# Performance work log

Hardware: AMD Instinct MI355X
Metric: run time of the kernel (lower is better)

Reference implementation:

```python
import jax, jax.numpy as jnp
import numpy as np

# Normalized wavelength grid for the 5 satellite bands (412.5, 442.5, 490, 510, 555 nm)
LAM_N = (jnp.array([412.5, 442.5, 490.0, 510.0, 555.0], dtype=jnp.float32) - 440.0) / 100.0
B1, B2, EPS, LR = 0.9, 0.999, 1e-8, 0.02  # Adam hyperparameters (torch defaults + lr)


def _optics(ch, pf):
    # ch: (B,3) log-concentrations [chla, nap, cdom]; pf: (14,) perturbation factors
    chla = jnp.exp(ch[:, 0:1])
    nap = jnp.exp(ch[:, 1:2])
    cdom = jnp.exp(ch[:, 2:3])
    a_ph = pf[0] * 0.05 * (1.0 + pf[1] * 0.1 * LAM_N + pf[2] * 0.01)       # (5,)
    a_cdom = pf[5] * 0.1 * jnp.exp(-pf[6] * 1.7 * LAM_N)                   # (5,)
    a = 0.0045 + a_ph * chla + a_cdom * cdom + pf[12] * 0.005 * nap        # (B,5)
    bb = 0.0012 + pf[3] * 0.001 * chla * (1.0 + pf[4] * 0.05 * LAM_N) + pf[13] * 0.005 * nap
    return a, bb


def _rrs(ch, X, pf):
    # Quadratic-in-u remote sensing reflectance model, modulated by direct/diffuse light split.
    a, bb = _optics(ch, pf)
    Edir, Edif = X[:, :, 0], X[:, :, 1]
    u = bb / (a + bb)
    rrs = (pf[7] * 0.089 + pf[8] * 0.1245 * u) * u
    return rrs * (Edir + 0.5 * Edif) / (Edir + Edif)  # (B,5)


def _kd(ch, X, pf):
    a, bb = _optics(ch, pf)
    mu = 0.5 + 0.5 * jax.nn.sigmoid(X[:, :, 3])  # mean cosine from zenith channel
    return (a + bb) / mu * (pf[9] * 0.9 + pf[10] * 0.1)  # (B,5)


def _bbp(ch, pf):
    chla = jnp.exp(ch[:, 0:1])
    nap = jnp.exp(ch[:, 1:2])
    lam3 = LAM_N[jnp.array([1, 2, 4])]  # bbp reported at 442.5, 490, 555 nm
    return pf[11] * (pf[3] * 0.001 * chla * (1.0 + pf[4] * 0.05 * lam3) + pf[13] * 0.005 * nap)


def _run(X, Y, chparam0, pf, x_a, s_a_inv, s_e_inv, num_iterations):
    def loss_fn(ch):
        r = _rrs(ch, X, pf) - Y                       # (B,5) data misfit
        d = ch - x_a                                  # (B,3) prior misfit
        return 0.5 * (jnp.einsum('bi,ij,bj->', r, s_e_inv, r)
                      + jnp.einsum('bi,ij,bj->', d, s_a_inv, d))

    @jax.checkpoint
    def step(carry, _):
        ch, m, v, t = carry
        g = jax.grad(loss_fn)(ch)
        t = t + 1.0
        m = B1 * m + (1.0 - B1) * g
        v = B2 * v + (1.0 - B2) * g * g
        mh = m / (1.0 - jnp.power(B1, t))
        vh = v / (1.0 - jnp.power(B2, t))
        ch = ch - LR * mh / (jnp.sqrt(vh) + EPS)
        return (ch, m, v, t), None

    ch0 = chparam0[:, 0, :]  # (B,3)
    z = jnp.zeros_like(ch0)
    (ch, _, _, _), _ = jax.lax.scan(step, (ch0, z, z, jnp.float32(0.0)), None, length=num_iterations)
    kd = _kd(ch, X, pf)
    bbp = _bbp(ch, pf)
    # output[:,0]=chla parameter, [:,1:6]=kd, [:,6:9]=bbp  (kind='parameter_estimation')
    return jnp.concatenate([ch[:, 0:1], kd, bbp], axis=1)  # (B,9)


def setup_inputs() -> dict:
    key = jax.random.key(0)
    k = jax.random.split(key, 3)
    B = 100000
    X = jax.random.uniform(k[0], (B, 5, 5), minval=0.1, maxval=1.0, dtype=jnp.float32)
    Y = jax.random.uniform(k[1], (B, 5), dtype=jnp.float32) * 0.01
    chparam0 = jax.random.normal(k[2], (B, 1, 3), dtype=jnp.float32) * 0.1
    perturbation_factors = jnp.ones((14,), dtype=jnp.float32)
    x_a = jnp.zeros((3,), dtype=jnp.float32)
    s_a_inv = jnp.eye(3, dtype=jnp.float32)
    s_e_inv = jnp.eye(5, dtype=jnp.float32) * 1e4
    return {"X": X, "Y": Y, "chparam0": chparam0,
            "perturbation_factors": perturbation_factors,
            "x_a": x_a, "s_a_inv": s_a_inv, "s_e_inv": s_e_inv,
            "num_iterations": 50}


def reference(X, Y, chparam0, perturbation_factors, x_a, s_a_inv, s_e_inv, num_iterations):
    return _run(X, Y, chparam0, perturbation_factors, x_a, s_a_inv, s_e_inv, num_iterations)
```

## Files before the change

### kernel.cpp

```cpp
#include <hip/hip_runtime.h>
#include <math.h>


typedef float v2f __attribute__((ext_vector_type(2)));

__device__ __forceinline__ float frcp(float x)  { return __builtin_amdgcn_rcpf(x); }
__device__ __forceinline__ float fsqrt_(float x){ return __builtin_amdgcn_sqrtf(x); }
__device__ __forceinline__ float fexp2_(float x){ return __builtin_amdgcn_exp2f(x); }
__device__ __forceinline__ float frsq_(float x) { return __builtin_amdgcn_rsqf(x); }
__device__ __forceinline__ float fexp(float x)  { return __expf(x); }

__device__ __forceinline__ v2f vrcp(v2f x){ v2f r; r.x = frcp(x.x); r.y = frcp(x.y); return r; }
__device__ __forceinline__ v2f vsqrt(v2f x){ v2f r; r.x = fsqrt_(x.x); r.y = fsqrt_(x.y); return r; }
__device__ __forceinline__ v2f vrsq(v2f x){ v2f r; r.x = frsq_(x.x); r.y = frsq_(x.y); return r; }
__device__ __forceinline__ v2f vexp(v2f x){ v2f r; r.x = fexp(x.x); r.y = fexp(x.y); return r; }
__device__ __forceinline__ v2f vexp_fast(v2f x){
    const v2f xs = x * 1.442695040888963f;
    v2f r; r.x = fexp2_(xs.x); r.y = fexp2_(xs.y); return r;
}
__device__ __forceinline__ v2f vminc(v2f x, float c){
    v2f r; r.x = fminf(x.x, c); r.y = fminf(x.y, c); return r;
}
__device__ __forceinline__ v2f bcast(float x){ v2f r; r.x = x; r.y = x; return r; }

__global__ __launch_bounds__(64)
void pe_kernel(const float* __restrict__ X,
               const float* __restrict__ Y,
               const float* __restrict__ ch0p,
               const float* __restrict__ pf,
               const float* __restrict__ x_a,
               const float* __restrict__ s_a_inv,
               const float* __restrict__ s_e_inv,
               const int*   __restrict__ n_iter,
               float* __restrict__ out,
               int B, int n0)
{
    const int b = blockIdx.x * blockDim.x + threadIdx.x;
    if (b >= n0) return;

    const bool valid1 = (b + n0) < B;
    const int e0 = b;
    const int e1 = valid1 ? (b + n0) : b;

    const float lam[5] = {-0.275f, 0.025f, 0.5f, 0.7f, 1.15f};

    float pfv[14];
#pragma unroll
    for (int i = 0; i < 14; ++i) pfv[i] = pf[i];

    const float xa0 = x_a[0], xa1 = x_a[1], xa2 = x_a[2];

    float Sa[3][3];
#pragma unroll
    for (int i = 0; i < 3; ++i)
#pragma unroll
        for (int j = 0; j < 3; ++j)
            Sa[i][j] = 0.5f * (s_a_inv[i*3+j] + s_a_inv[j*3+i]);

    float Se[5][5];
#pragma unroll
    for (int i = 0; i < 5; ++i)
#pragma unroll
        for (int j = 0; j < 5; ++j)
            Se[i][j] = 0.5f * (s_e_inv[i*5+j] + s_e_inv[j*5+i]);

    bool diag = true;
#pragma unroll
    for (int i = 0; i < 5; ++i)
#pragma unroll
        for (int j = 0; j < 5; ++j)
            if (i != j && Se[i][j] != 0.0f) diag = false;
#pragma unroll
    for (int i = 0; i < 3; ++i)
#pragma unroll
        for (int j = 0; j < 3; ++j)
            if (i != j && Sa[i][j] != 0.0f) diag = false;

    const int T = n_iter[0];

    const float A0   = 0.0045f, Bb0 = 0.0012f;
    const float Anap = pfv[12] * 0.005f;
    const float Bnap = pfv[13] * 0.005f;
    const float c1   = pfv[7] * 0.089f;
    const float c2   = pfv[8] * 0.1245f;
    const float c22  = 2.0f * c2;
    float Aph[5], Acd[5], Bph[5];
#pragma unroll
    for (int l = 0; l < 5; ++l) {
        Aph[l] = pfv[0] * 0.05f * (1.0f + pfv[1] * 0.1f * lam[l] + pfv[2] * 0.01f);
        Acd[l] = pfv[5] * 0.1f * fexp(-pfv[6] * 1.7f * lam[l]);
        Bph[l] = pfv[3] * 0.001f * (1.0f + pfv[4] * 0.05f * lam[l]);
    }

    v2f E[5], Yv[5], x3[5];
#pragma unroll
    for (int l = 0; l < 5; ++l) {
        const float Edir0 = X[e0*25 + l*5 + 0], Edir1 = X[e1*25 + l*5 + 0];
        const float Edif0 = X[e0*25 + l*5 + 1], Edif1 = X[e1*25 + l*5 + 1];
        x3[l].x = X[e0*25 + l*5 + 3];  x3[l].y = X[e1*25 + l*5 + 3];
        E[l].x  = (Edir0 + 0.5f * Edif0) * frcp(Edir0 + Edif0);
        E[l].y  = (Edir1 + 0.5f * Edif1) * frcp(Edir1 + Edif1);
        Yv[l].x = Y[e0*5 + l];  Yv[l].y = Y[e1*5 + l];
    }

    v2f ch[3], mm[3], vv[3];
#pragma unroll
    for (int k = 0; k < 3; ++k) {
        ch[k].x = ch0p[e0*3 + k];
        ch[k].y = ch0p[e1*3 + k];
        mm[k] = (v2f)0.0f;
        vv[k] = (v2f)0.0f;
    }

    float p1 = 1.0f, p2 = 1.0f;
    const float B1c = 0.9f,  oB1 = 1.0f - 0.9f;
    const float B2c = 0.999f, oB2 = 1.0f - 0.999f;
    const float LR = 0.02f, EPSc = 1e-8f;
    const float INV_EPS = 1e8f;

    if (diag) {
        const float SaD0 = Sa[0][0], SaD1 = Sa[1][1], SaD2 = Sa[2][2];
        const float ABn  = Anap + Bnap;
        const float AB0  = A0 + Bb0;

        v2f AB2[5], Bph2[5], Acd2[5], d3[5], d2[5], d1[5], d0[5];
        const float k3 = 2.0f * c2 * c2;
        const float k2 = 3.0f * c1 * c2;
        const float k1 = c1 * c1;
#pragma unroll
        for (int l = 0; l < 5; ++l) {
            AB2[l]  = bcast(Aph[l] + Bph[l]);
            Bph2[l] = bcast(Bph[l]);
            Acd2[l] = bcast(Acd[l]);
            const v2f E2S = (Se[l][l] * E[l]) * E[l];
            const v2f YES = (Se[l][l] * E[l]) * Yv[l];
            d3[l] = k3 * E2S;
            d2[l] = k2 * E2S;
            d1[l] = k1 * E2S - c22 * YES;
            d0[l] = -c1 * YES;
        }
        const v2f Bnapv = bcast(Bnap), ABnv = bcast(ABn);

        for (int t = 0; t < T; ++t) {
            p1 *= B1c; p2 *= B2c;
            const float lrim = LR * frcp(1.0f - p1);
            const float sqp2 = fsqrt_(1.0f - p2);

            const v2f chla = vexp_fast(ch[0]);
            const v2f nap  = vexp_fast(ch[1]);
            const v2f cdom = vexp_fast(ch[2]);

            const v2f bt = Bb0 + Bnap * nap;
            const v2f ct = AB0 + ABn  * nap;

            v2f sv[5], bbv[5];
#pragma unroll
            for (int l = 0; l < 5; ++l) {
                sv[l]  = AB2[l] * chla + (Acd2[l] * cdom + ct);
                bbv[l] = Bph2[l] * chla + bt;
            }

            const v2f P1 = sv[0] * sv[1];
            const v2f P2 = P1 * sv[2];
            const v2f P3 = P2 * sv[3];
            const v2f Pa = P3 * sv[4];
            const v2f S3 = sv[4] * sv[3];
            const v2f S2 = S3 * sv[2];
            const v2f S1 = S2 * sv[1];
            const v2f rP = vrcp(Pa);
            v2f inv[5];
            inv[0] = S1 * rP;
            inv[1] = (sv[0] * S2) * rP;
            inv[2] = (P1 * S3) * rP;
            inv[3] = (P2 * sv[4]) * rP;
            inv[4] = P3 * rP;

            v2f Ka = (v2f)0.0f, Kb = (v2f)0.0f;
            v2f KUa = (v2f)0.0f, KUb = (v2f)0.0f;
            v2f s0p = (v2f)0.0f, s0m = (v2f)0.0f;
            v2f s2a = (v2f)0.0f, s2b = (v2f)0.0f;
#pragma unroll
            for (int l = 0; l < 5; ++l) {
                const v2f u   = bbv[l] * inv[l];
                const v2f phi = ((d3[l] * u + d2[l]) * u + d1[l]) * u + d0[l];
                const v2f k   = inv[l] * phi;
                const v2f ku  = k * u;
                if ((l & 1) == 0) {
                    Ka  += k;
                    KUa += ku;
                    s2a += Acd2[l] * ku;
                } else {
                    Kb  += k;
                    KUb += ku;
                    s2b += Acd2[l] * ku;
                }
                s0p += Bph2[l] * k;
                s0m += AB2[l]  * ku;
            }
            const v2f K  = Ka + Kb;
            const v2f KU = KUa + KUb;
            const v2f s0 = s0p - s0m;
            const v2f s2 = s2a + s2b;
            const v2f s1 = Bnapv * K - ABnv * KU;

            v2f gs[3];
            gs[0] = SaD0 * (ch[0] - xa0) + chla * s0;
            gs[1] = SaD1 * (ch[1] - xa1) + nap  * s1;
            gs[2] = SaD2 * (ch[2] - xa2) - cdom * s2;

#pragma unroll
            for (int k = 0; k < 3; ++k) {
                const v2f g = gs[k];
                mm[k] = B1c * mm[k] + oB1 * g;
                vv[k] = B2c * vv[k] + oB2 * (g * g);
                const v2f dinv = vminc(vrsq(vv[k]) * sqp2, INV_EPS);
                ch[k] -= lrim * (mm[k] * dinv);
            }
        }
    } else {
        for (int t = 0; t < T; ++t) {
            p1 *= B1c; p2 *= B2c;
            const float im   = frcp(1.0f - p1);
            const float sqiv = fsqrt_(frcp(1.0f - p2));
            const float lrim = LR * im;

            const v2f chla = vexp(ch[0]);
            const v2f nap  = vexp(ch[1]);
            const v2f cdom = vexp(ch[2]);

            const v2f d0 = ch[0] - xa0, d1 = ch[1] - xa1, d2 = ch[2] - xa2;
            v2f g0 = Sa[0][0]*d0 + Sa[0][1]*d1 + Sa[0][2]*d2;
            v2f g1 = Sa[1][0]*d0 + Sa[1][1]*d1 + Sa[1][2]*d2;
            v2f g2 = Sa[2][0]*d0 + Sa[2][1]*d1 + Sa[2][2]*d2;

            const v2f da1 = Anap * nap;
            const v2f db1 = Bnap * nap;

            v2f av[5], bv[5], wv[5], rv[5];
#pragma unroll
            for (int l = 0; l < 5; ++l) {
                const v2f da0 = Aph[l] * chla;
                const v2f db0 = Bph[l] * chla;
                const v2f da2 = Acd[l] * cdom;
                const v2f a   = A0  + da0 + da2 + da1;
                const v2f bb  = Bb0 + db0 + db1;
                const v2f inv_s = vrcp(a + bb);
                const v2f u     = bb * inv_s;
                const v2f rrs   = (c1 + c2 * u) * u;
                av[l] = a;
                bv[l] = bb;
                rv[l] = rrs * E[l] - Yv[l];
                wv[l] = (c1 + c22 * u) * E[l] * inv_s * inv_s;
            }

            v2f s0 = (v2f)0.0f, s1 = (v2f)0.0f, s2 = (v2f)0.0f;
#pragma unroll
            for (int i = 0; i < 5; ++i) {
                const v2f q = Se[i][0]*rv[0] + Se[i][1]*rv[1] + Se[i][2]*rv[2]
                            + Se[i][3]*rv[3] + Se[i][4]*rv[4];
                const v2f h = wv[i] * q;
                s0 += h * (Bph[i] * av[i] - Aph[i] * bv[i]);
                s1 += h * (Bnap   * av[i] - Anap   * bv[i]);
                s2 += h * (Acd[i] * bv[i]);
            }
            g0 += chla * s0;
            g1 += nap  * s1;
            g2 -= cdom * s2;

            const v2f gs[3] = {g0, g1, g2};
#pragma unroll
            for (int k = 0; k < 3; ++k) {
                const v2f g = gs[k];
                mm[k] = B1c * mm[k] + oB1 * g;
                vv[k] = B2c * vv[k] + oB2 * (g * g);
                const v2f den = vsqrt(vv[k]) * sqiv + EPSc;
                ch[k] -= (lrim * mm[k]) * vrcp(den);
            }
        }
    }

    const float kdscale = pfv[9] * 0.9f + pfv[10] * 0.1f;
    const float lam3[3] = {0.025f, 0.5f, 1.15f};

    const v2f chla = vexp(ch[0]);
    const v2f nap  = vexp(ch[1]);
    const v2f cdom = vexp(ch[2]);

#pragma unroll
    for (int ee = 0; ee < 2; ++ee) {
        if (ee == 1 && !valid1) break;
        const int e = ee ? e1 : e0;
        const float chl = ee ? chla.y : chla.x;
        const float np  = ee ? nap.y  : nap.x;
        const float cd  = ee ? cdom.y : cdom.x;

        float o[9];
        o[0] = ee ? ch[0].y : ch[0].x;
#pragma unroll
        for (int l = 0; l < 5; ++l) {
            const float a  = A0  + Aph[l]*chl + Acd[l]*cd + Anap*np;
            const float bb = Bb0 + Bph[l]*chl + Bnap*np;
            const float xx = ee ? x3[l].y : x3[l].x;
            const float sig = frcp(1.0f + fexp(-xx));
            const float mu  = 0.5f + 0.5f * sig;
            o[1 + l] = (a + bb) * frcp(mu) * kdscale;
        }
#pragma unroll
        for (int j = 0; j < 3; ++j) {
            const float bph = pfv[3] * 0.001f * (1.0f + pfv[4] * 0.05f * lam3[j]);
            o[6 + j] = pfv[11] * (bph * chl + Bnap * np);
        }
#pragma unroll
        for (int i = 0; i < 9; ++i) out[e*9 + i] = o[i];
    }
}

extern "C" void kernel_launch(void* const* d_in, const int* in_sizes, int n_in,
                              void* d_out, int out_size, void* d_ws, size_t ws_size,
                              hipStream_t stream) {
    const float* X   = (const float*)d_in[0];
    const float* Y   = (const float*)d_in[1];
    const float* ch0 = (const float*)d_in[2];
    const float* pf  = (const float*)d_in[3];
    const float* xa  = (const float*)d_in[4];
    const float* sa  = (const float*)d_in[5];
    const float* se  = (const float*)d_in[6];
    const int*   ni  = (const int*)d_in[7];
    float* out = (float*)d_out;

    const int B  = in_sizes[0] / 25;
    const int n0 = (B + 1) / 2;
    const int block = 64;
    const int grid = (n0 + block - 1) / block;
    hipLaunchKernelGGL(pe_kernel, dim3(grid), dim3(block), 0, stream,
                       X, Y, ch0, pf, xa, sa, se, ni, out, B, n0);
}
```

Before: 93.90 us.

## Precompute Adam bias-correction table, work in log2 domain, vectorize loads/stores

Builds a per-block shared-memory table of per-step Adam bias-correction scalars (folding lr, sqrt and eps clamp), and keeps the concentration state in a log2-scaled domain so the exp2 calls need no per-step multiply. It also simplifies the gradient accumulation, folds the prior term constants, and uses wider vector loads for X/Y/ch0 and vector stores for the output. This aims to cut per-iteration scalar ALU and transcendental work and the number of memory instructions. In exchange it adds an LDS table build plus a barrier at kernel start, and the unaligned vector accesses rely on 4-byte-aligned vector types.

```diff
diff --git a/kernel.cpp b/kernel.cpp
--- a/kernel.cpp
+++ b/kernel.cpp
@@ -3,6 +3,8 @@
 
 
 typedef float v2f __attribute__((ext_vector_type(2)));
+typedef float f4a __attribute__((ext_vector_type(4), aligned(4)));
+typedef float f2a __attribute__((ext_vector_type(2), aligned(4)));
 
 __device__ __forceinline__ float frcp(float x)  { return __builtin_amdgcn_rcpf(x); }
 __device__ __forceinline__ float fsqrt_(float x){ return __builtin_amdgcn_sqrtf(x); }
@@ -14,14 +16,12 @@
 __device__ __forceinline__ v2f vsqrt(v2f x){ v2f r; r.x = fsqrt_(x.x); r.y = fsqrt_(x.y); return r; }
 __device__ __forceinline__ v2f vrsq(v2f x){ v2f r; r.x = frsq_(x.x); r.y = frsq_(x.y); return r; }
 __device__ __forceinline__ v2f vexp(v2f x){ v2f r; r.x = fexp(x.x); r.y = fexp(x.y); return r; }
-__device__ __forceinline__ v2f vexp_fast(v2f x){
-    const v2f xs = x * 1.442695040888963f;
-    v2f r; r.x = fexp2_(xs.x); r.y = fexp2_(xs.y); return r;
-}
+__device__ __forceinline__ v2f vexp2(v2f x){ v2f r; r.x = fexp2_(x.x); r.y = fexp2_(x.y); return r; }
 __device__ __forceinline__ v2f vminc(v2f x, float c){
     v2f r; r.x = fminf(x.x, c); r.y = fminf(x.y, c); return r;
 }
-__device__ __forceinline__ v2f bcast(float x){ v2f r; r.x = x; r.y = x; return r; }
+
+#define TBL_N 512
 
 __global__ __launch_bounds__(64)
 void pe_kernel(const float* __restrict__ X,
@@ -35,13 +35,54 @@
                float* __restrict__ out,
                int B, int n0)
 {
-    const int b = blockIdx.x * blockDim.x + threadIdx.x;
-    if (b >= n0) return;
-
+    __shared__ f2a tab[TBL_N];
+
+    const int bt = blockIdx.x * blockDim.x + threadIdx.x;
+    const bool active = (bt < n0);
+    const int b = active ? bt : 0;
     const bool valid1 = (b + n0) < B;
     const int e0 = b;
     const int e1 = valid1 ? (b + n0) : b;
 
+    f4a xr0[5], xr1[5];
+    const float* xb0 = X + (size_t)e0 * 25;
+    const float* xb1 = X + (size_t)e1 * 25;
+#pragma unroll
+    for (int l = 0; l < 5; ++l) {
+        xr0[l] = *reinterpret_cast<const f4a*>(xb0 + l * 5);
+        xr1[l] = *reinterpret_cast<const f4a*>(xb1 + l * 5);
+    }
+    const f4a y40 = *reinterpret_cast<const f4a*>(Y + (size_t)e0 * 5);
+    const f4a y41 = *reinterpret_cast<const f4a*>(Y + (size_t)e1 * 5);
+    const float y4e0 = Y[(size_t)e0 * 5 + 4];
+    const float y4e1 = Y[(size_t)e1 * 5 + 4];
+    const f2a c010 = *reinterpret_cast<const f2a*>(ch0p + (size_t)e0 * 3);
+    const f2a c011 = *reinterpret_cast<const f2a*>(ch0p + (size_t)e1 * 3);
+    const float c2e0 = ch0p[(size_t)e0 * 3 + 2];
+    const float c2e1 = ch0p[(size_t)e1 * 3 + 2];
+
+    const int T = n_iter[0];
+
+    const float LAM2E  = 1.4426950408889634f;
+    const float INVL2E = 0.6931471805599453f;
+    const float LRc = 0.02f;
+    const float LRL = LRc * LAM2E;
+    const float LN999 = -0.0010004874458f;
+
+    {
+        const int tn = (T < TBL_N) ? T : TBL_N;
+        for (int t = (int)threadIdx.x; t < tn; t += 64) {
+            const float tf = (float)(t + 1);
+            const float p1t = __powf(0.9f, tf);
+            const float om2 = -expm1f(tf * LN999);
+            const float im  = LRL * frcp(1.0f - p1t);
+            f2a e; e.x = im * fsqrt_(om2); e.y = im * 1e8f;
+            tab[t] = e;
+        }
+    }
+    __syncthreads();
+    if (!active) return;
+
     const float lam[5] = {-0.275f, 0.025f, 0.5f, 0.7f, 1.15f};
 
     float pfv[14];
@@ -75,8 +116,6 @@
 #pragma unroll
         for (int j = 0; j < 3; ++j)
             if (i != j && Sa[i][j] != 0.0f) diag = false;
-
-    const int T = n_iter[0];
 
     const float A0   = 0.0045f, Bb0 = 0.0012f;
     const float Anap = pfv[12] * 0.005f;
@@ -95,43 +134,47 @@
     v2f E[5], Yv[5], x3[5];
 #pragma unroll
     for (int l = 0; l < 5; ++l) {
-        const float Edir0 = X[e0*25 + l*5 + 0], Edir1 = X[e1*25 + l*5 + 0];
-        const float Edif0 = X[e0*25 + l*5 + 1], Edif1 = X[e1*25 + l*5 + 1];
-        x3[l].x = X[e0*25 + l*5 + 3];  x3[l].y = X[e1*25 + l*5 + 3];
-        E[l].x  = (Edir0 + 0.5f * Edif0) * frcp(Edir0 + Edif0);
-        E[l].y  = (Edir1 + 0.5f * Edif1) * frcp(Edir1 + Edif1);
-        Yv[l].x = Y[e0*5 + l];  Yv[l].y = Y[e1*5 + l];
+        const float Ed0 = xr0[l].x, Ef0 = xr0[l].y;
+        const float Ed1 = xr1[l].x, Ef1 = xr1[l].y;
+        x3[l].x = xr0[l].w;  x3[l].y = xr1[l].w;
+        E[l].x  = (Ed0 + 0.5f * Ef0) * frcp(Ed0 + Ef0);
+        E[l].y  = (Ed1 + 0.5f * Ef1) * frcp(Ed1 + Ef1);
+        Yv[l].x = (l < 4) ? y40[l] : y4e0;
+        Yv[l].y = (l < 4) ? y41[l] : y4e1;
     }
 
     v2f ch[3], mm[3], vv[3];
-#pragma unroll
-    for (int k = 0; k < 3; ++k) {
-        ch[k].x = ch0p[e0*3 + k];
-        ch[k].y = ch0p[e1*3 + k];
-        mm[k] = (v2f)0.0f;
-        vv[k] = (v2f)0.0f;
-    }
-
-    float p1 = 1.0f, p2 = 1.0f;
-    const float B1c = 0.9f,  oB1 = 1.0f - 0.9f;
+    ch[0].x = c010.x;  ch[0].y = c011.x;
+    ch[1].x = c010.y;  ch[1].y = c011.y;
+    ch[2].x = c2e0;    ch[2].y = c2e1;
+#pragma unroll
+    for (int k = 0; k < 3; ++k) { mm[k] = (v2f)0.0f; vv[k] = (v2f)0.0f; }
+
+    const float B1c = 0.9f,   oB1 = 1.0f - 0.9f;
     const float B2c = 0.999f, oB2 = 1.0f - 0.999f;
-    const float LR = 0.02f, EPSc = 1e-8f;
-    const float INV_EPS = 1e8f;
+    const float EPSc = 1e-8f;
+
+    v2f chla, nap, cdom;
 
     if (diag) {
+        ch[0] *= LAM2E;  ch[1] *= LAM2E;  ch[2] *= LAM2E;
+
         const float SaD0 = Sa[0][0], SaD1 = Sa[1][1], SaD2 = Sa[2][2];
+        const float SaD0i = SaD0 * INVL2E, SaD1i = SaD1 * INVL2E, SaD2i = SaD2 * INVL2E;
+        const float cxa0 = SaD0 * xa0, cxa1 = SaD1 * xa1, cxa2 = SaD2 * xa2;
         const float ABn  = Anap + Bnap;
-        const float AB0  = A0 + Bb0;
-
-        v2f AB2[5], Bph2[5], Acd2[5], d3[5], d2[5], d1[5], d0[5];
+        const float AB0c = A0 + Bb0;
+
+        float AB2s[5], Bph2s[5], Acd2s[5];
+        v2f d3[5], d2[5], d1[5], d0[5];
         const float k3 = 2.0f * c2 * c2;
         const float k2 = 3.0f * c1 * c2;
         const float k1 = c1 * c1;
 #pragma unroll
         for (int l = 0; l < 5; ++l) {
-            AB2[l]  = bcast(Aph[l] + Bph[l]);
-            Bph2[l] = bcast(Bph[l]);
-            Acd2[l] = bcast(Acd[l]);
+            AB2s[l]  = Aph[l] + Bph[l];
+            Bph2s[l] = Bph[l];
+            Acd2s[l] = Acd[l];
             const v2f E2S = (Se[l][l] * E[l]) * E[l];
             const v2f YES = (Se[l][l] * E[l]) * Yv[l];
             d3[l] = k3 * E2S;
@@ -139,25 +182,32 @@
             d1[l] = k1 * E2S - c22 * YES;
             d0[l] = -c1 * YES;
         }
-        const v2f Bnapv = bcast(Bnap), ABnv = bcast(ABn);
 
         for (int t = 0; t < T; ++t) {
-            p1 *= B1c; p2 *= B2c;
-            const float lrim = LR * frcp(1.0f - p1);
-            const float sqp2 = fsqrt_(1.0f - p2);
-
-            const v2f chla = vexp_fast(ch[0]);
-            const v2f nap  = vexp_fast(ch[1]);
-            const v2f cdom = vexp_fast(ch[2]);
-
-            const v2f bt = Bb0 + Bnap * nap;
-            const v2f ct = AB0 + ABn  * nap;
+            float Asc, Csc;
+            if (t < TBL_N) {
+                const f2a ac = tab[t];
+                Asc = ac.x; Csc = ac.y;
+            } else {
+                const float tf = (float)(t + 1);
+                const float p1t = __powf(0.9f, tf);
+                const float om2 = -expm1f(tf * LN999);
+                const float im  = LRL * frcp(1.0f - p1t);
+                Asc = im * fsqrt_(om2); Csc = im * 1e8f;
+            }
+
+            const v2f xch = vexp2(ch[0]);
+            const v2f xnp = vexp2(ch[1]);
+            const v2f xcd = vexp2(ch[2]);
+
+            const v2f btv = Bb0  + Bnap * xnp;
+            const v2f ctv = AB0c + ABn  * xnp;
 
             v2f sv[5], bbv[5];
 #pragma unroll
             for (int l = 0; l < 5; ++l) {
-                sv[l]  = AB2[l] * chla + (Acd2[l] * cdom + ct);
-                bbv[l] = Bph2[l] * chla + bt;
+                sv[l]  = AB2s[l] * xch + (Acd2s[l] * xcd + ctv);
+                bbv[l] = Bph2s[l] * xch + btv;
             }
 
             const v2f P1 = sv[0] * sv[1];
@@ -175,73 +225,68 @@
             inv[3] = (P2 * sv[4]) * rP;
             inv[4] = P3 * rP;
 
-            v2f Ka = (v2f)0.0f, Kb = (v2f)0.0f;
-            v2f KUa = (v2f)0.0f, KUb = (v2f)0.0f;
             v2f s0p = (v2f)0.0f, s0m = (v2f)0.0f;
-            v2f s2a = (v2f)0.0f, s2b = (v2f)0.0f;
+            v2f s1a = (v2f)0.0f, s1b = (v2f)0.0f;
+            v2f s2v = (v2f)0.0f;
 #pragma unroll
             for (int l = 0; l < 5; ++l) {
                 const v2f u   = bbv[l] * inv[l];
                 const v2f phi = ((d3[l] * u + d2[l]) * u + d1[l]) * u + d0[l];
                 const v2f k   = inv[l] * phi;
                 const v2f ku  = k * u;
-                if ((l & 1) == 0) {
-                    Ka  += k;
-                    KUa += ku;
-                    s2a += Acd2[l] * ku;
-                } else {
-                    Kb  += k;
-                    KUb += ku;
-                    s2b += Acd2[l] * ku;
-                }
-                s0p += Bph2[l] * k;
-                s0m += AB2[l]  * ku;
-            }
-            const v2f K  = Ka + Kb;
-            const v2f KU = KUa + KUb;
+                s0p += Bph2s[l] * k;
+                s0m += AB2s[l]  * ku;
+                s1a += Bnap * k;
+                s1b += ABn  * ku;
+                s2v += Acd2s[l] * ku;
+            }
             const v2f s0 = s0p - s0m;
-            const v2f s2 = s2a + s2b;
-            const v2f s1 = Bnapv * K - ABnv * KU;
+            const v2f s1 = s1a - s1b;
 
             v2f gs[3];
-            gs[0] = SaD0 * (ch[0] - xa0) + chla * s0;
-            gs[1] = SaD1 * (ch[1] - xa1) + nap  * s1;
-            gs[2] = SaD2 * (ch[2] - xa2) - cdom * s2;
+            gs[0] = SaD0i * ch[0] + (xch * s0 - cxa0);
+            gs[1] = SaD1i * ch[1] + (xnp * s1 - cxa1);
+            gs[2] = SaD2i * ch[2] - (xcd * s2v + cxa2);
 
 #pragma unroll
             for (int k = 0; k < 3; ++k) {
                 const v2f g = gs[k];
                 mm[k] = B1c * mm[k] + oB1 * g;
                 vv[k] = B2c * vv[k] + oB2 * (g * g);
-                const v2f dinv = vminc(vrsq(vv[k]) * sqp2, INV_EPS);
-                ch[k] -= lrim * (mm[k] * dinv);
-            }
-        }
+                const v2f dv = vminc(vrsq(vv[k]) * Asc, Csc);
+                ch[k] -= mm[k] * dv;
+            }
+        }
+
+        chla = vexp2(ch[0]);  nap = vexp2(ch[1]);  cdom = vexp2(ch[2]);
+        ch[0] *= INVL2E;
     } else {
+        float p1 = 1.0f, p2 = 1.0f;
+        const float LR = 0.02f;
         for (int t = 0; t < T; ++t) {
             p1 *= B1c; p2 *= B2c;
             const float im   = frcp(1.0f - p1);
             const float sqiv = fsqrt_(frcp(1.0f - p2));
             const float lrim = LR * im;
 
-            const v2f chla = vexp(ch[0]);
-            const v2f nap  = vexp(ch[1]);
-            const v2f cdom = vexp(ch[2]);
-
-            const v2f d0 = ch[0] - xa0, d1 = ch[1] - xa1, d2 = ch[2] - xa2;
-            v2f g0 = Sa[0][0]*d0 + Sa[0][1]*d1 + Sa[0][2]*d2;
-            v2f g1 = Sa[1][0]*d0 + Sa[1][1]*d1 + Sa[1][2]*d2;
-            v2f g2 = Sa[2][0]*d0 + Sa[2][1]*d1 + Sa[2][2]*d2;
-
-            const v2f da1 = Anap * nap;
-            const v2f db1 = Bnap * nap;
+            const v2f chl = vexp(ch[0]);
+            const v2f np  = vexp(ch[1]);
+            const v2f cd  = vexp(ch[2]);
+
+            const v2f dd0 = ch[0] - xa0, dd1 = ch[1] - xa1, dd2 = ch[2] - xa2;
+            v2f g0 = Sa[0][0]*dd0 + Sa[0][1]*dd1 + Sa[0][2]*dd2;
+            v2f g1 = Sa[1][0]*dd0 + Sa[1][1]*dd1 + Sa[1][2]*dd2;
+            v2f g2 = Sa[2][0]*dd0 + Sa[2][1]*dd1 + Sa[2][2]*dd2;
+
+            const v2f da1 = Anap * np;
+            const v2f db1 = Bnap * np;
 
             v2f av[5], bv[5], wv[5], rv[5];
 #pragma unroll
             for (int l = 0; l < 5; ++l) {
-                const v2f da0 = Aph[l] * chla;
-                const v2f db0 = Bph[l] * chla;
-                const v2f da2 = Acd[l] * cdom;
+                const v2f da0 = Aph[l] * chl;
+                const v2f db0 = Bph[l] * chl;
+                const v2f da2 = Acd[l] * cd;
                 const v2f a   = A0  + da0 + da2 + da1;
                 const v2f bb  = Bb0 + db0 + db1;
                 const v2f inv_s = vrcp(a + bb);
@@ -263,28 +308,25 @@
                 s1 += h * (Bnap   * av[i] - Anap   * bv[i]);
                 s2 += h * (Acd[i] * bv[i]);
             }
-            g0 += chla * s0;
-            g1 += nap  * s1;
-            g2 -= cdom * s2;
-
-            const v2f gs[3] = {g0, g1, g2};
+            g0 += chl * s0;
+            g1 += np  * s1;
+            g2 -= cd  * s2;
+
+            const v2f gsv[3] = {g0, g1, g2};
 #pragma unroll
             for (int k = 0; k < 3; ++k) {
-                const v2f g = gs[k];
+                const v2f g = gsv[k];
                 mm[k] = B1c * mm[k] + oB1 * g;
                 vv[k] = B2c * vv[k] + oB2 * (g * g);
                 const v2f den = vsqrt(vv[k]) * sqiv + EPSc;
                 ch[k] -= (lrim * mm[k]) * vrcp(den);
             }
         }
+        chla = vexp(ch[0]);  nap = vexp(ch[1]);  cdom = vexp(ch[2]);
     }
 
     const float kdscale = pfv[9] * 0.9f + pfv[10] * 0.1f;
     const float lam3[3] = {0.025f, 0.5f, 1.15f};
-
-    const v2f chla = vexp(ch[0]);
-    const v2f nap  = vexp(ch[1]);
-    const v2f cdom = vexp(ch[2]);
 
 #pragma unroll
     for (int ee = 0; ee < 2; ++ee) {
@@ -310,8 +352,12 @@
             const float bph = pfv[3] * 0.001f * (1.0f + pfv[4] * 0.05f * lam3[j]);
             o[6 + j] = pfv[11] * (bph * chl + Bnap * np);
         }
-#pragma unroll
-        for (int i = 0; i < 9; ++i) out[e*9 + i] = o[i];
+        f4a w0, w1;
+        w0.x = o[0]; w0.y = o[1]; w0.z = o[2]; w0.w = o[3];
+        w1.x = o[4]; w1.y = o[5]; w1.z = o[6]; w1.w = o[7];
+        *reinterpret_cast<f4a*>(out + (size_t)e*9)     = w0;
+        *reinterpret_cast<f4a*>(out + (size_t)e*9 + 4) = w1;
+        out[(size_t)e*9 + 8] = o[8];
     }
 }
 
```

Result: no change. 93.68 us (-0.2%).
